# Optimization experiments

Measured on AMD Instinct MI355X. Metric: run time of the kernel, lower is better.

The kernel has to match this reference:

```python
import jax, jax.numpy as jnp
import numpy as np

L = 2          # loopnum
BS = 64        # batch
T = 512        # tracklength
EC = 1024      # ecnum
CA1 = 1024     # ca1num
CA3 = 1024     # ca3num
ACT = 2        # actnum
TS = 0.1
SIGMA = 5.0    # ca3sigma


def setup_inputs() -> dict:
    key = jax.random.key(0)
    ks = jax.random.split(key, 10)
    return {
        "cue_ec3input": jax.random.normal(ks[0], (BS, T, EC), dtype=jnp.float32),
        "ec3_last": jax.random.uniform(ks[1], (L, BS, EC), dtype=jnp.float32),
        "ec5_last": jax.random.uniform(ks[2], (L, BS, EC), dtype=jnp.float32),
        "ca1_last": jax.random.uniform(ks[3], (L, BS, CA1), dtype=jnp.float32),
        # per-loop parameters, stacked on leading loop axis (mirrors nn.ModuleList)
        "wca3ca1": jax.random.uniform(ks[4], (L, CA3, CA1), dtype=jnp.float32) * 0.01,
        "wec3ca1": jax.random.normal(ks[5], (L, EC, CA1), dtype=jnp.float32) * 0.03,   # ~xavier scale
        "wca1ec5": jax.random.normal(ks[6], (L, CA1, EC), dtype=jnp.float32) * 0.03,
        "ca1bias": jnp.zeros((L, CA1), dtype=jnp.float32),
        "ec5bias": jnp.zeros((L, EC), dtype=jnp.float32),
        # interLayer i: nn.Linear(ca1num, ecnum) -> weight (EC, CA1), bias (EC,)
        "inter_w": jax.random.normal(ks[7], (L, EC, CA1), dtype=jnp.float32) * 0.02,
        "inter_b": jnp.zeros((L, EC), dtype=jnp.float32),
        "wca1act": jax.random.normal(ks[8], (CA1, ACT), dtype=jnp.float32) * 0.03,
        "actbias": jnp.zeros((ACT,), dtype=jnp.float32),
    }


def reference(cue_ec3input, ec3_last, ec5_last, ca1_last,
              wca3ca1, wec3ca1, wca1ec5, ca1bias, ec5bias,
              inter_w, inter_b, wca1act, actbias):
    ca3center = jnp.linspace(0.0, float(T), CA3)          # (CA3,)
    positions = jnp.arange(T, dtype=jnp.float32)          # (T,)
    cue_t = jnp.swapaxes(cue_ec3input, 0, 1)              # (T, BS, EC)

    def step(carry, xin):
        ec3, ec5, ca1 = carry                             # each (L, BS, dim)
        x, cue_x = xin                                    # scalar, (BS, EC)
        ca3 = jnp.exp(-(ca3center - x) ** 2 / (2.0 * SIGMA ** 2))  # (CA3,)
        ec3input = cue_x
        new_ec3, new_ec5, new_ca1 = [], [], []
        for i in range(L):                                # fixed, structurally distinct loops
            ca1_i = jax.nn.relu(
                jax.nn.sigmoid(10.0 * (ca3 @ wca3ca1[i] - 0.5))           # (CA1,)
                * (1.0 + 3.0 * jax.nn.sigmoid(ec3[i] @ wec3ca1[i]))       # (BS, CA1)
                - ca1bias[i]
            )
            ec5_i = ec5[i] + 10.0 * TS * (ca1_i @ wca1ec5[i]) + ec5bias[i]
            ec5_i = 0.69 + 0.3 * jax.nn.sigmoid(4.0 * (ec5_i - 0.3))
            ec3_i = ec5_i * ec3[i] + 0.6 * ec3input
            ec3input = ca1_i @ inter_w[i].T + inter_b[i]  # feed next loop
            new_ec3.append(ec3_i); new_ec5.append(ec5_i); new_ca1.append(ca1_i)
        ec3 = jnp.stack(new_ec3); ec5 = jnp.stack(new_ec5); ca1 = jnp.stack(new_ca1)
        # histories record batch element 0 only, as in the original
        hist = (ec3[:, 0, :], ec5[:, 0, :], ca1[:, 0, :])
        return (ec3, ec5, ca1), hist

    (ec3, ec5, ca1), (ec3his, ec5his, ca1his) = jax.lax.scan(
        step, (ec3_last, ec5_last, ca1_last), (positions, cue_t))

    # scan stacks on axis 0 -> (T, L, dim); original layout is (L, T, dim)
    ec3his = jnp.swapaxes(ec3his, 0, 1)
    ec5his = jnp.swapaxes(ec5his, 0, 1)
    ca1his = jnp.swapaxes(ca1his, 0, 1)

    actCell = ca1[-1] @ wca1act + actbias                 # (BS, ACT)
    return actCell, ec3his, ec5his, ca1his
```

## Files before the change

kernel.cpp:

```cpp
#include <hip/hip_runtime.h>

#define Lnum 2
#define BSn  64
#define Tn   512
#define ECn  1024
#define CA1n 1024

typedef short bf16x8 __attribute__((ext_vector_type(8)));
typedef float f32x4  __attribute__((ext_vector_type(4)));

#define MFMA16(a,b,c) __builtin_amdgcn_mfma_f32_16x16x32_bf16((a),(b),(c),0,0,0)

#define OUT_E3  128
#define OUT_E5  (128 + Lnum*Tn*ECn)
#define OUT_CA1 (128 + 2*Lnum*Tn*ECn)

#define WS_EC3B 0
#define WS_CA1B 262144
#define WS_EC5F 524288
#define WS_EC3F 1048576
#define WS_CA1L 1572864
#define WS_S    1835008
#define WS_W1T  3932160
#define WS_W2T  8126464
#define WS_W3T  12320768

__device__ __forceinline__ float sigm(float x) { return 1.0f / (1.0f + __expf(-x)); }

__device__ __forceinline__ short f2bf(float f) {
  unsigned u = __float_as_uint(f);
  u += 0x7fffu + ((u >> 16) & 1u);
  return (short)(u >> 16);
}
__device__ __forceinline__ float bf2f(short s) {
  return __uint_as_float(((unsigned)(unsigned short)s) << 16);
}


__global__ void prep_state(const float* __restrict__ ec3_last,
                           const float* __restrict__ ec5_last,
                           short* __restrict__ ec3b,
                           float* __restrict__ ec5f, float* __restrict__ ec3f) {
  int i = blockIdx.x * blockDim.x + threadIdx.x;
  float v3 = ec3_last[i];
  ec3b[i] = f2bf(v3);
  ec3f[i] = v3;
  ec5f[i] = ec5_last[i];
}

__global__ void prep_wt(const float* __restrict__ w1, const float* __restrict__ w2,
                        short* __restrict__ w1t, short* __restrict__ w2t) {
  __shared__ float tile[64][65];
  const int b = blockIdx.x;
  const int m  = b >> 9;
  const int li = (b >> 8) & 1;
  const int kt = (b >> 4) & 15;
  const int ct = b & 15;
  const float* src = (m == 0 ? w1 : w2) + li * (1024 * 1024);
  short* dst = (m == 0 ? w1t : w2t) + li * (1024 * 1024);
#pragma unroll
  for (int i = 0; i < 16; ++i) {
    int idx = threadIdx.x + i * 256;
    int r = idx >> 6, c = idx & 63;
    tile[r][c] = src[(kt * 64 + r) * 1024 + ct * 64 + c];
  }
  __syncthreads();
#pragma unroll
  for (int i = 0; i < 16; ++i) {
    int idx = threadIdx.x + i * 256;
    int c = idx >> 6, r = idx & 63;
    dst[(ct * 64 + c) * 1024 + kt * 64 + r] = f2bf(tile[r][c]);
  }
}

__global__ void prep_w3(const float* __restrict__ inter_w, short* __restrict__ w3t) {
  int i = blockIdx.x * blockDim.x + threadIdx.x;
  w3t[i] = f2bf(inter_w[i]);
}

__global__ void prep_ca3(const float* __restrict__ wca3ca1, short* __restrict__ S) {
  const int t = blockIdx.x >> 1, li = blockIdx.x & 1;
  __shared__ float gauss[192];
  const float stepc = 512.0f / 1023.0f;
  const float tf = (float)t;
  int kmin = (int)floorf((tf - 40.0f) / stepc) - 1; if (kmin < 0) kmin = 0;
  int kmax = (int)ceilf((tf + 40.0f) / stepc) + 1;  if (kmax > 1023) kmax = 1023;
  int nw = kmax - kmin + 1;
  for (int j = threadIdx.x; j < nw; j += 256) {
    float d = (float)(kmin + j) * stepc - tf;
    gauss[j] = __expf(-d * d * 0.02f);
  }
  __syncthreads();
  const float* W = wca3ca1 + li * (1024 * 1024);
  for (int c = threadIdx.x; c < 1024; c += 256) {
    float s = 0.0f;
    for (int j = 0; j < nw; ++j) s += gauss[j] * W[(kmin + j) * 1024 + c];
    S[(li * Tn + t) * 1024 + c] = f2bf(sigm(10.0f * (s - 0.5f)));
  }
}


__global__ void __launch_bounds__(128) phaseA(
    const short* __restrict__ ec3b, const short* __restrict__ w1t,
    const short* __restrict__ stab, const float* __restrict__ ca1bias,
    short* __restrict__ ca1b, float* __restrict__ ca1l,
    float* __restrict__ out, int t) {
  const int b = blockIdx.x;
  const int mh = b >> 7, li = (b >> 6) & 1, c0 = (b & 63) << 4;
  const int tid = threadIdx.x;
  const int lane = tid & 63, wave = tid >> 6;
  const int fr = lane & 15, ks = lane >> 4;
  const int r0 = (mh * 2 + wave) << 4;
  const short* A = ec3b + li * 65536 + (r0 + fr) * 1024 + ks * 8;
  const short* B = w1t + li * 1048576 + (c0 + fr) * 1024 + ks * 8;
  f32x4 a0 = {0.f,0.f,0.f,0.f}, a1 = {0.f,0.f,0.f,0.f};
#pragma unroll
  for (int kk = 0; kk < 16; ++kk) {
    a0 = MFMA16(*(const bf16x8*)(A + kk * 32),       *(const bf16x8*)(B + kk * 32),       a0);
    a1 = MFMA16(*(const bf16x8*)(A + 512 + kk * 32), *(const bf16x8*)(B + 512 + kk * 32), a1);
  }
  f32x4 acc = a0 + a1;
  const int ccol = c0 + fr;
  const float g  = bf2f(stab[(li * Tn + t) * 1024 + ccol]);
  const float cb = ca1bias[li * 1024 + ccol];
#pragma unroll
  for (int r = 0; r < 4; ++r) {
    int grow = r0 + ks * 4 + r;
    float cv = fmaxf(g * (1.0f + 3.0f * sigm(acc[r])) - cb, 0.0f);
    ca1b[li * 65536 + grow * 1024 + ccol] = f2bf(cv);
    if (grow == 0) out[OUT_CA1 + (li * Tn + t) * 1024 + ccol] = cv;
    if (t == Tn - 1 && li == 1) ca1l[grow * 1024 + ccol] = cv;
  }
}

__global__ void __launch_bounds__(128) phaseB(
    const short* __restrict__ ca1b, const short* __restrict__ w2t,
    const short* __restrict__ w3t, const float* __restrict__ cue,
    const float* __restrict__ ec5bias, const float* __restrict__ interb,
    float* __restrict__ ec5f, float* __restrict__ ec3f,
    short* __restrict__ ec3b, float* __restrict__ out, int t) {
  const int b = blockIdx.x;
  const int mh = b >> 7, li = (b >> 6) & 1, e0 = (b & 63) << 4;
  const int tid = threadIdx.x;
  const int lane = tid & 63, wave = tid >> 6;
  const int fr = lane & 15, ks = lane >> 4;
  const int r0 = (mh * 2 + wave) << 4;
  const short* A2 = ca1b + li * 65536 + (r0 + fr) * 1024 + ks * 8;
  const short* B2 = w2t + li * 1048576 + (e0 + fr) * 1024 + ks * 8;
  const int ecol = e0 + fr;

  f32x4 p0 = {0.f,0.f,0.f,0.f}, p1 = {0.f,0.f,0.f,0.f};
#pragma unroll
  for (int kk = 0; kk < 16; ++kk) {
    p0 = MFMA16(*(const bf16x8*)(A2 + kk * 32),       *(const bf16x8*)(B2 + kk * 32),       p0);
    p1 = MFMA16(*(const bf16x8*)(A2 + 512 + kk * 32), *(const bf16x8*)(B2 + 512 + kk * 32), p1);
  }
  f32x4 g2 = p0 + p1;

  f32x4 xin;
  if (li == 1) {
    const short* A3 = ca1b + (r0 + fr) * 1024 + ks * 8;
    const short* B3 = w3t + (e0 + fr) * 1024 + ks * 8;
    f32x4 q0 = {0.f,0.f,0.f,0.f}, q1 = {0.f,0.f,0.f,0.f};
#pragma unroll
    for (int kk = 0; kk < 16; ++kk) {
      q0 = MFMA16(*(const bf16x8*)(A3 + kk * 32),       *(const bf16x8*)(B3 + kk * 32),       q0);
      q1 = MFMA16(*(const bf16x8*)(A3 + 512 + kk * 32), *(const bf16x8*)(B3 + 512 + kk * 32), q1);
    }
    f32x4 q = q0 + q1;
    float ib = interb[ecol];
#pragma unroll
    for (int r = 0; r < 4; ++r) xin[r] = q[r] + ib;
  } else {
#pragma unroll
    for (int r = 0; r < 4; ++r)
      xin[r] = cue[((r0 + ks * 4 + r) * Tn + t) * 1024 + ecol];
  }

  const float e5b = ec5bias[li * 1024 + ecol];
#pragma unroll
  for (int r = 0; r < 4; ++r) {
    int grow = r0 + ks * 4 + r;
    int sidx = li * 65536 + grow * 1024 + ecol;
    float raw = ec5f[sidx] + g2[r] + e5b;
    float e5 = 0.69f + 0.3f * sigm(4.0f * (raw - 0.3f));
    ec5f[sidx] = e5;
    float e3 = e5 * ec3f[sidx] + 0.6f * xin[r];
    ec3f[sidx] = e3;
    ec3b[sidx] = f2bf(e3);
    if (grow == 0) {
      out[OUT_E5 + (li * Tn + t) * 1024 + ecol] = e5;
      out[OUT_E3 + (li * Tn + t) * 1024 + ecol] = e3;
    }
  }
}

__global__ void act_cell(const float* __restrict__ ca1l, const float* __restrict__ wca1act,
                         const float* __restrict__ actbias, float* __restrict__ out) {
  int tid = threadIdx.x;
  if (tid < 128) {
    int b = tid >> 1, a = tid & 1;
    float s = 0.0f;
    for (int k = 0; k < 1024; ++k) s += ca1l[b * 1024 + k] * wca1act[k * 2 + a];
    out[b * 2 + a] = s + actbias[a];
  }
}

extern "C" void kernel_launch(void* const* d_in, const int* in_sizes, int n_in,
                              void* d_out, int out_size, void* d_ws, size_t ws_size,
                              hipStream_t stream) {
  (void)in_sizes; (void)n_in; (void)out_size; (void)ws_size;
  const float* cue      = (const float*)d_in[0];
  const float* ec3_last = (const float*)d_in[1];
  const float* ec5_last = (const float*)d_in[2];
  const float* wca3ca1  = (const float*)d_in[4];
  const float* wec3ca1  = (const float*)d_in[5];
  const float* wca1ec5  = (const float*)d_in[6];
  const float* ca1bias  = (const float*)d_in[7];
  const float* ec5bias  = (const float*)d_in[8];
  const float* inter_w  = (const float*)d_in[9];
  const float* inter_b  = (const float*)d_in[10];
  const float* wca1act  = (const float*)d_in[11];
  const float* actbias  = (const float*)d_in[12];
  float* out = (float*)d_out;

  char* ws = (char*)d_ws;
  short* ec3b = (short*)(ws + WS_EC3B);
  short* ca1b = (short*)(ws + WS_CA1B);
  float* ec5f = (float*)(ws + WS_EC5F);
  float* ec3f = (float*)(ws + WS_EC3F);
  float* ca1l = (float*)(ws + WS_CA1L);
  short* stab = (short*)(ws + WS_S);
  short* w1t  = (short*)(ws + WS_W1T);
  short* w2t  = (short*)(ws + WS_W2T);
  short* w3t  = (short*)(ws + WS_W3T);

  prep_state<<<dim3(512), dim3(256), 0, stream>>>(ec3_last, ec5_last, ec3b, ec5f, ec3f);
  prep_wt<<<dim3(1024), dim3(256), 0, stream>>>(wec3ca1, wca1ec5, w1t, w2t);
  prep_w3<<<dim3(4096), dim3(256), 0, stream>>>(inter_w, w3t);
  prep_ca3<<<dim3(1024), dim3(256), 0, stream>>>(wca3ca1, stab);

  for (int t = 0; t < Tn; ++t) {
    phaseA<<<dim3(256), dim3(128), 0, stream>>>(ec3b, w1t, stab, ca1bias, ca1b, ca1l, out, t);
    phaseB<<<dim3(256), dim3(128), 0, stream>>>(ca1b, w2t, w3t, cue, ec5bias, inter_b,
                                                ec5f, ec3f, ec3b, out, t);
  }

  act_cell<<<dim3(1), dim3(128), 0, stream>>>(ca1l, wca1act, actbias, out);
}
```

Measured before the change: 8.320 ms.

## Fuse per-step phase kernels into persistent chunked kernel with software grid barrier

Replaces the 1024 per-timestep phaseA/phaseB launches with 32 launches of a persistent 128-block kernel. Each launch runs 16 timesteps and separates the phases with a flag-based grid barrier. The ec5/ec3 state stays in registers across a chunk, and bf16 activations are exchanged as packed 32-bit words through agent-scope atomic loads and stores. This removes kernel-launch overhead and the state round-trips through memory. The cost is fewer blocks per phase, spin-waiting, and a reliance on all 128 blocks being co-resident to avoid deadlock.

```diff
diff --git a/kernel.cpp b/kernel.cpp
--- a/kernel.cpp
+++ b/kernel.cpp
@@ -5,6 +5,7 @@
 #define Tn   512
 #define ECn  1024
 #define CA1n 1024
+#define CHUNK 16
 
 typedef short bf16x8 __attribute__((ext_vector_type(8)));
 typedef float f32x4  __attribute__((ext_vector_type(4)));
@@ -15,37 +16,56 @@
 #define OUT_E5  (128 + Lnum*Tn*ECn)
 #define OUT_CA1 (128 + 2*Lnum*Tn*ECn)
 
-#define WS_EC3B 0
-#define WS_CA1B 262144
-#define WS_EC5F 524288
-#define WS_EC3F 1048576
-#define WS_CA1L 1572864
-#define WS_S    1835008
-#define WS_W1T  3932160
-#define WS_W2T  8126464
-#define WS_W3T  12320768
+#define WS_FLAGS 0
+#define WS_EC3U  8192
+#define WS_CA1U  270336
+#define WS_EC5F  532480
+#define WS_EC3F  1056768
+#define WS_CA1L  1581056
+#define WS_S     1843200
+#define WS_W1T   3940352
+#define WS_W2T   8134656
+#define WS_W3T   12328960
+
+#define AST(p, v) __hip_atomic_store((p), (v), __ATOMIC_RELAXED, __HIP_MEMORY_SCOPE_AGENT)
+#define ALD(p)    __hip_atomic_load((p), __ATOMIC_RELAXED, __HIP_MEMORY_SCOPE_AGENT)
 
 __device__ __forceinline__ float sigm(float x) { return 1.0f / (1.0f + __expf(-x)); }
 
-__device__ __forceinline__ short f2bf(float f) {
+__device__ __forceinline__ unsigned f2bfu(float f) {
   unsigned u = __float_as_uint(f);
   u += 0x7fffu + ((u >> 16) & 1u);
-  return (short)(u >> 16);
-}
+  return u >> 16;
+}
+__device__ __forceinline__ short f2bf(float f) { return (short)f2bfu(f); }
 __device__ __forceinline__ float bf2f(short s) {
   return __uint_as_float(((unsigned)(unsigned short)s) << 16);
 }
 
+__device__ __forceinline__ bf16x8 loadA(const unsigned* p) {
+  union { unsigned u[4]; bf16x8 b; } x;
+  unsigned* q = (unsigned*)p;
+  x.u[0] = ALD(q + 0);
+  x.u[1] = ALD(q + 1);
+  x.u[2] = ALD(q + 2);
+  x.u[3] = ALD(q + 3);
+  return x.b;
+}
+
 
 __global__ void prep_state(const float* __restrict__ ec3_last,
                            const float* __restrict__ ec5_last,
-                           short* __restrict__ ec3b,
+                           unsigned* __restrict__ flags, unsigned* __restrict__ ec3u,
                            float* __restrict__ ec5f, float* __restrict__ ec3f) {
   int i = blockIdx.x * blockDim.x + threadIdx.x;
+  if (i < 2048) flags[i] = 0u;
   float v3 = ec3_last[i];
-  ec3b[i] = f2bf(v3);
   ec3f[i] = v3;
   ec5f[i] = ec5_last[i];
+  if (i < Lnum * BSn * 512) {
+    float lo = ec3_last[2 * i], hi = ec3_last[2 * i + 1];
+    ec3u[i] = f2bfu(lo) | (f2bfu(hi) << 16);
+  }
 }
 
 __global__ void prep_wt(const float* __restrict__ w1, const float* __restrict__ w2,
@@ -99,99 +119,140 @@
   }
 }
 
-
-__global__ void __launch_bounds__(128) phaseA(
-    const short* __restrict__ ec3b, const short* __restrict__ w1t,
-    const short* __restrict__ stab, const float* __restrict__ ca1bias,
-    short* __restrict__ ca1b, float* __restrict__ ca1l,
-    float* __restrict__ out, int t) {
+__device__ __forceinline__ void gridbar(unsigned* flags, unsigned target) {
+  asm volatile("s_waitcnt vmcnt(0)" ::: "memory");
+  __syncthreads();
+  if (threadIdx.x == 0) AST(&flags[blockIdx.x * 16], target);
+  if (threadIdx.x < 128) {
+    while (ALD(&flags[threadIdx.x * 16]) < target) {}
+  }
+  __builtin_amdgcn_sched_barrier(0);
+  __syncthreads();
+}
+
+__global__ void __launch_bounds__(256, 1) stepchunk(
+    const float* __restrict__ cue,
+    const short* __restrict__ w1t, const short* __restrict__ w2t,
+    const short* __restrict__ w3t, const short* __restrict__ stab,
+    const float* __restrict__ ca1bias, const float* __restrict__ ec5bias,
+    const float* __restrict__ interb,
+    unsigned* __restrict__ flags, unsigned* __restrict__ ec3u,
+    unsigned* __restrict__ ca1u, float* __restrict__ ec5f, float* __restrict__ ec3f,
+    float* __restrict__ ca1l, float* __restrict__ out, int t0, int base) {
   const int b = blockIdx.x;
-  const int mh = b >> 7, li = (b >> 6) & 1, c0 = (b & 63) << 4;
+  const int li = b >> 6;
+  const int c0 = (b & 63) << 4;
   const int tid = threadIdx.x;
   const int lane = tid & 63, wave = tid >> 6;
   const int fr = lane & 15, ks = lane >> 4;
-  const int r0 = (mh * 2 + wave) << 4;
-  const short* A = ec3b + li * 65536 + (r0 + fr) * 1024 + ks * 8;
-  const short* B = w1t + li * 1048576 + (c0 + fr) * 1024 + ks * 8;
-  f32x4 a0 = {0.f,0.f,0.f,0.f}, a1 = {0.f,0.f,0.f,0.f};
-#pragma unroll
-  for (int kk = 0; kk < 16; ++kk) {
-    a0 = MFMA16(*(const bf16x8*)(A + kk * 32),       *(const bf16x8*)(B + kk * 32),       a0);
-    a1 = MFMA16(*(const bf16x8*)(A + 512 + kk * 32), *(const bf16x8*)(B + 512 + kk * 32), a1);
-  }
-  f32x4 acc = a0 + a1;
+  const int r0 = wave << 4;
   const int ccol = c0 + fr;
-  const float g  = bf2f(stab[(li * Tn + t) * 1024 + ccol]);
-  const float cb = ca1bias[li * 1024 + ccol];
+
+  const unsigned* A1u = ec3u + li * 32768 + (r0 + fr) * 512 + ks * 4;
+  const unsigned* A2u = ca1u + li * 32768 + (r0 + fr) * 512 + ks * 4;
+  const unsigned* A3u = ca1u + (r0 + fr) * 512 + ks * 4;
+  const short* B1 = w1t + li * 1048576 + ccol * 1024 + ks * 8;
+  const short* B2 = w2t + li * 1048576 + ccol * 1024 + ks * 8;
+  const short* B3 = w3t + ccol * 1024 + ks * 8;
+
+  const float cb  = ca1bias[li * 1024 + ccol];
+  const float e5b = ec5bias[li * 1024 + ccol];
+  const float ib0 = interb[1024 + ccol];
+
+  float e5r[4], e3r[4];
 #pragma unroll
   for (int r = 0; r < 4; ++r) {
-    int grow = r0 + ks * 4 + r;
-    float cv = fmaxf(g * (1.0f + 3.0f * sigm(acc[r])) - cb, 0.0f);
-    ca1b[li * 65536 + grow * 1024 + ccol] = f2bf(cv);
-    if (grow == 0) out[OUT_CA1 + (li * Tn + t) * 1024 + ccol] = cv;
-    if (t == Tn - 1 && li == 1) ca1l[grow * 1024 + ccol] = cv;
-  }
-}
-
-__global__ void __launch_bounds__(128) phaseB(
-    const short* __restrict__ ca1b, const short* __restrict__ w2t,
-    const short* __restrict__ w3t, const float* __restrict__ cue,
-    const float* __restrict__ ec5bias, const float* __restrict__ interb,
-    float* __restrict__ ec5f, float* __restrict__ ec3f,
-    short* __restrict__ ec3b, float* __restrict__ out, int t) {
-  const int b = blockIdx.x;
-  const int mh = b >> 7, li = (b >> 6) & 1, e0 = (b & 63) << 4;
-  const int tid = threadIdx.x;
-  const int lane = tid & 63, wave = tid >> 6;
-  const int fr = lane & 15, ks = lane >> 4;
-  const int r0 = (mh * 2 + wave) << 4;
-  const short* A2 = ca1b + li * 65536 + (r0 + fr) * 1024 + ks * 8;
-  const short* B2 = w2t + li * 1048576 + (e0 + fr) * 1024 + ks * 8;
-  const int ecol = e0 + fr;
-
-  f32x4 p0 = {0.f,0.f,0.f,0.f}, p1 = {0.f,0.f,0.f,0.f};
-#pragma unroll
-  for (int kk = 0; kk < 16; ++kk) {
-    p0 = MFMA16(*(const bf16x8*)(A2 + kk * 32),       *(const bf16x8*)(B2 + kk * 32),       p0);
-    p1 = MFMA16(*(const bf16x8*)(A2 + 512 + kk * 32), *(const bf16x8*)(B2 + 512 + kk * 32), p1);
-  }
-  f32x4 g2 = p0 + p1;
-
-  f32x4 xin;
-  if (li == 1) {
-    const short* A3 = ca1b + (r0 + fr) * 1024 + ks * 8;
-    const short* B3 = w3t + (e0 + fr) * 1024 + ks * 8;
-    f32x4 q0 = {0.f,0.f,0.f,0.f}, q1 = {0.f,0.f,0.f,0.f};
-#pragma unroll
-    for (int kk = 0; kk < 16; ++kk) {
-      q0 = MFMA16(*(const bf16x8*)(A3 + kk * 32),       *(const bf16x8*)(B3 + kk * 32),       q0);
-      q1 = MFMA16(*(const bf16x8*)(A3 + 512 + kk * 32), *(const bf16x8*)(B3 + 512 + kk * 32), q1);
+    int sidx = li * 65536 + (r0 + ks * 4 + r) * 1024 + ccol;
+    e5r[r] = ec5f[sidx];
+    e3r[r] = ec3f[sidx];
+  }
+
+  unsigned tgt = (unsigned)base;
+
+  for (int tt = 0; tt < CHUNK; ++tt) {
+    const int t = t0 + tt;
+
+    float cueq[4];
+    if (li == 0) {
+#pragma unroll
+      for (int r = 0; r < 4; ++r)
+        cueq[r] = cue[((r0 + ks * 4 + r) * Tn + t) * 1024 + ccol];
     }
-    f32x4 q = q0 + q1;
-    float ib = interb[ecol];
-#pragma unroll
-    for (int r = 0; r < 4; ++r) xin[r] = q[r] + ib;
-  } else {
-#pragma unroll
-    for (int r = 0; r < 4; ++r)
-      xin[r] = cue[((r0 + ks * 4 + r) * Tn + t) * 1024 + ecol];
-  }
-
-  const float e5b = ec5bias[li * 1024 + ecol];
+
+    {
+      f32x4 a0 = {0.f,0.f,0.f,0.f}, a1 = {0.f,0.f,0.f,0.f};
+#pragma unroll
+      for (int kk = 0; kk < 16; ++kk) {
+        a0 = MFMA16(loadA(A1u + kk * 16),       *(const bf16x8*)(B1 + kk * 32),       a0);
+        a1 = MFMA16(loadA(A1u + 256 + kk * 16), *(const bf16x8*)(B1 + 512 + kk * 32), a1);
+      }
+      f32x4 acc = a0 + a1;
+      const float g = bf2f(stab[(li * Tn + t) * 1024 + ccol]);
+#pragma unroll
+      for (int r = 0; r < 4; ++r) {
+        int grow = r0 + ks * 4 + r;
+        float cv = fmaxf(g * (1.0f + 3.0f * sigm(acc[r])) - cb, 0.0f);
+        unsigned my = f2bfu(cv);
+        unsigned pr = (unsigned)__shfl_xor((int)my, 1);
+        if ((fr & 1) == 0)
+          AST(ca1u + li * 32768 + grow * 512 + ((c0 + fr) >> 1), my | (pr << 16));
+        if (grow == 0) out[OUT_CA1 + (li * Tn + t) * 1024 + ccol] = cv;
+        if (t == Tn - 1 && li == 1) ca1l[grow * 1024 + ccol] = cv;
+      }
+    }
+    gridbar(flags, ++tgt);
+
+    {
+      f32x4 p0 = {0.f,0.f,0.f,0.f}, p1 = {0.f,0.f,0.f,0.f};
+#pragma unroll
+      for (int kk = 0; kk < 16; ++kk) {
+        p0 = MFMA16(loadA(A2u + kk * 16),       *(const bf16x8*)(B2 + kk * 32),       p0);
+        p1 = MFMA16(loadA(A2u + 256 + kk * 16), *(const bf16x8*)(B2 + 512 + kk * 32), p1);
+      }
+      f32x4 g2 = p0 + p1;
+
+      f32x4 xin;
+      if (li == 1) {
+        f32x4 q0 = {0.f,0.f,0.f,0.f}, q1 = {0.f,0.f,0.f,0.f};
+#pragma unroll
+        for (int kk = 0; kk < 16; ++kk) {
+          q0 = MFMA16(loadA(A3u + kk * 16),       *(const bf16x8*)(B3 + kk * 32),       q0);
+          q1 = MFMA16(loadA(A3u + 256 + kk * 16), *(const bf16x8*)(B3 + 512 + kk * 32), q1);
+        }
+        f32x4 q = q0 + q1;
+#pragma unroll
+        for (int r = 0; r < 4; ++r) xin[r] = q[r] + ib0;
+      } else {
+#pragma unroll
+        for (int r = 0; r < 4; ++r) xin[r] = cueq[r];
+      }
+
+#pragma unroll
+      for (int r = 0; r < 4; ++r) {
+        int grow = r0 + ks * 4 + r;
+        float raw = e5r[r] + g2[r] + e5b;
+        float e5 = 0.69f + 0.3f * sigm(4.0f * (raw - 0.3f));
+        e5r[r] = e5;
+        float e3 = e5 * e3r[r] + 0.6f * xin[r];
+        e3r[r] = e3;
+        unsigned my = f2bfu(e3);
+        unsigned pr = (unsigned)__shfl_xor((int)my, 1);
+        if ((fr & 1) == 0)
+          AST(ec3u + li * 32768 + grow * 512 + ((c0 + fr) >> 1), my | (pr << 16));
+        if (grow == 0) {
+          out[OUT_E5 + (li * Tn + t) * 1024 + ccol] = e5;
+          out[OUT_E3 + (li * Tn + t) * 1024 + ccol] = e3;
+        }
+      }
+    }
+    gridbar(flags, ++tgt);
+  }
+
 #pragma unroll
   for (int r = 0; r < 4; ++r) {
-    int grow = r0 + ks * 4 + r;
-    int sidx = li * 65536 + grow * 1024 + ecol;
-    float raw = ec5f[sidx] + g2[r] + e5b;
-    float e5 = 0.69f + 0.3f * sigm(4.0f * (raw - 0.3f));
-    ec5f[sidx] = e5;
-    float e3 = e5 * ec3f[sidx] + 0.6f * xin[r];
-    ec3f[sidx] = e3;
-    ec3b[sidx] = f2bf(e3);
-    if (grow == 0) {
-      out[OUT_E5 + (li * Tn + t) * 1024 + ecol] = e5;
-      out[OUT_E3 + (li * Tn + t) * 1024 + ecol] = e3;
-    }
+    int sidx = li * 65536 + (r0 + ks * 4 + r) * 1024 + ccol;
+    ec5f[sidx] = e5r[r];
+    ec3f[sidx] = e3r[r];
   }
 }
 
@@ -225,8 +286,9 @@
   float* out = (float*)d_out;
 
   char* ws = (char*)d_ws;
-  short* ec3b = (short*)(ws + WS_EC3B);
-  short* ca1b = (short*)(ws + WS_CA1B);
+  unsigned* flags = (unsigned*)(ws + WS_FLAGS);
+  unsigned* ec3u  = (unsigned*)(ws + WS_EC3U);
+  unsigned* ca1u  = (unsigned*)(ws + WS_CA1U);
   float* ec5f = (float*)(ws + WS_EC5F);
   float* ec3f = (float*)(ws + WS_EC3F);
   float* ca1l = (float*)(ws + WS_CA1L);
@@ -235,15 +297,15 @@
   short* w2t  = (short*)(ws + WS_W2T);
   short* w3t  = (short*)(ws + WS_W3T);
 
-  prep_state<<<dim3(512), dim3(256), 0, stream>>>(ec3_last, ec5_last, ec3b, ec5f, ec3f);
+  prep_state<<<dim3(512), dim3(256), 0, stream>>>(ec3_last, ec5_last, flags, ec3u, ec5f, ec3f);
   prep_wt<<<dim3(1024), dim3(256), 0, stream>>>(wec3ca1, wca1ec5, w1t, w2t);
   prep_w3<<<dim3(4096), dim3(256), 0, stream>>>(inter_w, w3t);
   prep_ca3<<<dim3(1024), dim3(256), 0, stream>>>(wca3ca1, stab);
 
-  for (int t = 0; t < Tn; ++t) {
-    phaseA<<<dim3(256), dim3(128), 0, stream>>>(ec3b, w1t, stab, ca1bias, ca1b, ca1l, out, t);
-    phaseB<<<dim3(256), dim3(128), 0, stream>>>(ca1b, w2t, w3t, cue, ec5bias, inter_b,
-                                                ec5f, ec3f, ec3b, out, t);
+  for (int c = 0; c < Tn / CHUNK; ++c) {
+    stepchunk<<<dim3(128), dim3(256), 0, stream>>>(
+        cue, w1t, w2t, w3t, stab, ca1bias, ec5bias, inter_b,
+        flags, ec3u, ca1u, ec5f, ec3f, ca1l, out, c * CHUNK, c * 2 * CHUNK);
   }
 
   act_cell<<<dim3(1), dim3(128), 0, stream>>>(ca1l, wca1act, actbias, out);
```

Measured after the change: 27.48 ms. +230.3%, slower.
